# Optimization experiments

Hardware: AMD Instinct MI355X
Metric: run time of the kernel (lower is better)

## Reference

```python
import jax, jax.numpy as jnp
import numpy as np

B, S, D = 4, 2048, 2048
E = 8            # num_experts
TOP_K = 2
H = 1408         # intermediate_size per expert
SH = 2 * H       # shared expert intermediate (shared_experts=2)


def setup_inputs() -> dict:
    key = jax.random.key(0)
    ks = jax.random.split(key, 8)
    sc = 0.02
    return {
        "hidden_states": jax.random.normal(ks[0], (B, S, D), jnp.float32),
        "gate_w": jax.random.normal(ks[1], (E, D), jnp.float32) * sc,   # torch Linear weight [out,in]
        "w1": jax.random.normal(ks[2], (E, H, D), jnp.float32) * sc,    # gate_proj per expert
        "w3": jax.random.normal(ks[3], (E, H, D), jnp.float32) * sc,    # up_proj per expert
        "w2": jax.random.normal(ks[4], (E, D, H), jnp.float32) * sc,    # down_proj per expert
        "sw1": jax.random.normal(ks[5], (SH, D), jnp.float32) * sc,
        "sw3": jax.random.normal(ks[6], (SH, D), jnp.float32) * sc,
        "sw2": jax.random.normal(ks[7], (D, SH), jnp.float32) * sc,
    }


def reference(hidden_states, gate_w, w1, w3, w2, sw1, sw3, sw2):
    b, s, d = hidden_states.shape
    x = hidden_states.reshape(-1, d)                      # [T, D]
    logits = x @ gate_w.T                                 # [T, E]
    rw, sel = jax.lax.top_k(logits, TOP_K)                # [T, K]
    rw = jax.nn.softmax(rw, axis=-1)                      # norm_topk_prob=True
    onehot = jax.nn.one_hot(sel, E, dtype=x.dtype)        # [T, K, E]
    token_mask = onehot.sum(axis=1)                       # [T, E] in {0,1}
    # NOTE: faithful to the source quirk: expert_weights.sum(dim=-1) on a flat
    # masked gather sums routing weights over ALL tokens selecting the expert,
    # producing one scalar per expert.
    s_e = (rw[..., None] * onehot).sum(axis=(0, 1))       # [E]
    combine = token_mask * s_e                            # [T, E]
    # per-expert SwiGLU MLP on all tokens (dense combine form of gather/scatter)
    g = jnp.einsum('td,ehd->eth', x, w1)                  # [E, T, H]
    u = jnp.einsum('td,ehd->eth', x, w3)
    a = jax.nn.silu(g) * u
    y = jnp.einsum('eth,edh->etd', a, w2)                 # [E, T, D]
    out = jnp.einsum('te,etd->td', combine, y)            # [T, D]
    shared = (jax.nn.silu(x @ sw1.T) * (x @ sw3.T)) @ sw2.T
    out = out + shared
    return out.reshape(b, s, d)
```

## Files before the change

### kernel.cpp

```cpp
#include <hip/hip_runtime.h>
#include <hip/hip_bf16.h>
#include <stdint.h>

#define T_TOK 8192
#define DIM   2048
#define NEXP  8
#define HDIM  1408
#define SHDIM 2816

typedef __attribute__((ext_vector_type(8))) short bfrag;
typedef __attribute__((ext_vector_type(4))) float f32x4;

__device__ __forceinline__ short f2bf(float f) {
    union { float f; uint32_t u; } v; v.f = f;
    return (short)((v.u + 0x8000u) >> 16);
}

__device__ __forceinline__ bfrag cvt8(float4 a, float4 b) {
    bfrag r;
    r[0] = f2bf(a.x); r[1] = f2bf(a.y); r[2] = f2bf(a.z); r[3] = f2bf(a.w);
    r[4] = f2bf(b.x); r[5] = f2bf(b.y); r[6] = f2bf(b.z); r[7] = f2bf(b.w);
    return r;
}

__device__ __forceinline__ void gload16(const void* g, void* l) {
    __builtin_amdgcn_global_load_lds(
        (__attribute__((address_space(1))) void*)(g),
        (__attribute__((address_space(3))) void*)(l), 16, 0, 0);
}

#define MFMA16(a, b, c) __builtin_amdgcn_mfma_f32_16x16x32_bf16((a), (b), (c), 0, 0, 0)


__global__ __launch_bounds__(256) void gate_kernel(
    const float* __restrict__ x, const float* __restrict__ gw,
    int* __restrict__ sel, int* __restrict__ meta, float* __restrict__ s_e)
{
    __shared__ float g[NEXP * DIM];
    for (int i = threadIdx.x; i < NEXP * DIM; i += 256) g[i] = gw[i];
    __syncthreads();
    const int wid = threadIdx.x >> 6, lane = threadIdx.x & 63;
    for (int it = 0; it < 8; ++it) {
        const int t = blockIdx.x * 32 + wid * 8 + it;
        float acc[NEXP];
#pragma unroll
        for (int e = 0; e < NEXP; ++e) acc[e] = 0.f;
        const float4* xr = (const float4*)(x + (size_t)t * DIM);
        for (int j = 0; j < DIM / 4; j += 64) {
            float4 xv = xr[j + lane];
#pragma unroll
            for (int e = 0; e < NEXP; ++e) {
                float4 gv = *(const float4*)&g[e * DIM + (j + lane) * 4];
                acc[e] += xv.x * gv.x + xv.y * gv.y + xv.z * gv.z + xv.w * gv.w;
            }
        }
#pragma unroll
        for (int e = 0; e < NEXP; ++e)
            for (int o = 32; o; o >>= 1) acc[e] += __shfl_xor(acc[e], o);
        if (lane == 0) {
            int e0 = 0; float v0 = acc[0];
#pragma unroll
            for (int e = 1; e < NEXP; ++e) if (acc[e] > v0) { v0 = acc[e]; e0 = e; }
            int e1 = -1; float v1 = -3.4e38f;
#pragma unroll
            for (int e = 0; e < NEXP; ++e) if (e != e0 && acc[e] > v1) { v1 = acc[e]; e1 = e; }
            float p0 = 1.f / (1.f + __expf(v1 - v0));
            float p1 = 1.f - p0;
            sel[2 * t] = e0; sel[2 * t + 1] = e1;
            atomicAdd(&s_e[e0], p0); atomicAdd(&s_e[e1], p1);
            atomicAdd(&meta[e0], 1); atomicAdd(&meta[e1], 1);
        }
    }
}

__global__ void scan_kernel(int* meta) {
    if (threadIdx.x == 0) {
        int acc = 0;
        for (int e = 0; e < NEXP; ++e) {
            meta[16 + e] = acc;
            meta[8 + e]  = acc;
            acc += meta[e];
        }
        meta[24] = acc;
    }
}

__global__ __launch_bounds__(256) void fill_kernel(
    const int* __restrict__ sel, int* __restrict__ meta, int* __restrict__ list)
{
    const int t = blockIdx.x * 256 + threadIdx.x;
    int e0 = sel[2 * t], e1 = sel[2 * t + 1];
    int p0 = atomicAdd(&meta[8 + e0], 1); list[p0] = t;
    int p1 = atomicAdd(&meta[8 + e1], 1); list[p1] = t;
}

__global__ __launch_bounds__(256) void cvt_kernel(
    const float* __restrict__ in, __hip_bfloat16* __restrict__ out, int n8)
{
    int i = blockIdx.x * 256 + threadIdx.x;
    const int stride = gridDim.x * 256;
    for (; i < n8; i += stride) {
        const float4* p = (const float4*)(in + (size_t)i * 8);
        float4 a = p[0], b = p[1];
        *(bfrag*)(out + (size_t)i * 8) = cvt8(a, b);
    }
}


template<int N, bool GATHER>
__global__ __launch_bounds__(512, 2) void up_v3(
    const __hip_bfloat16* __restrict__ X,
    const __hip_bfloat16* __restrict__ W1,
    const __hip_bfloat16* __restrict__ W3,
    __hip_bfloat16* __restrict__ act,
    const int* __restrict__ list,
    const int* __restrict__ meta)
{
    constexpr int K = DIM;
    constexpr int NT = K / 64;
    constexpr int nx = N / 128, ny = T_TOK / 256, nz = GATHER ? NEXP : 1;
    constexpr int nwg = nx * ny * nz, cpx = nwg / 8;
    const int bid = (int)blockIdx.x + nx * ((int)blockIdx.y + ny * (int)blockIdx.z);
    const int virt = (bid & 7) * cpx + (bid >> 3);
    const int xi = virt % nx;
    const int rest = virt / nx;
    const int yi = rest % ny;
    const int e = rest / ny;

    int count, base;
    if (GATHER) {
        count = meta[e]; base = meta[16 + e];
        if (yi * 256 >= count) return;
    } else { count = T_TOK; base = 0; }
    const int m0 = yi * 256, n0 = xi * 128;

    __shared__ alignas(16) short As[2][256 * 64];
    __shared__ alignas(16) short B1s[2][128 * 64];
    __shared__ alignas(16) short B3s[2][128 * 64];

    const int tid = threadIdx.x, wid = tid >> 6, lane = tid & 63;
    const int rlo = lane >> 3;
    const int swslot = (lane & 7) ^ rlo;

    const __hip_bfloat16* pA[4];
#pragma unroll
    for (int q = 0; q < 4; ++q) {
        int row = (q * 8 + wid) * 8 + rlo;
        int r = m0 + row; if (r > count - 1) r = count - 1;
        int ga = GATHER ? list[base + r] : r;
        pA[q] = X + (size_t)ga * K + swslot * 8;
    }
    const __hip_bfloat16* pB1[2];
    const __hip_bfloat16* pB3[2];
#pragma unroll
    for (int q = 0; q < 2; ++q) {
        int row = (q * 8 + wid) * 8 + rlo;
        pB1[q] = W1 + ((size_t)e * N + n0 + row) * K + swslot * 8;
        pB3[q] = W3 + ((size_t)e * N + n0 + row) * K + swslot * 8;
    }

#define STAGE_UP(T, BUF) do { const int k0_ = (T) * 64;                         \
    _Pragma("unroll") for (int q = 0; q < 4; ++q)                               \
        gload16(pA[q] + k0_, &As[BUF][(q * 8 + wid) * 512]);                    \
    _Pragma("unroll") for (int q = 0; q < 2; ++q) {                             \
        gload16(pB1[q] + k0_, &B1s[BUF][(q * 8 + wid) * 512]);                  \
        gload16(pB3[q] + k0_, &B3s[BUF][(q * 8 + wid) * 512]); } } while (0)

    const int wm = wid >> 2, wn = wid & 3;
    const int l15 = lane & 15, lhi = lane >> 4;

    f32x4 accg[8][2], accu[8][2];
#pragma unroll
    for (int i = 0; i < 8; ++i)
#pragma unroll
        for (int j = 0; j < 2; ++j) { accg[i][j] = 0.f; accu[i][j] = 0.f; }

    STAGE_UP(0, 0);
    __syncthreads();
    int cur = 0;
#pragma unroll 1
    for (int t = 0; t < NT; ++t) {
        if (t + 1 < NT) STAGE_UP(t + 1, cur ^ 1);
        __builtin_amdgcn_sched_barrier(0);
        bfrag b1f[2][2], b3f[2][2];
#pragma unroll
        for (int j = 0; j < 2; ++j)
#pragma unroll
            for (int kk = 0; kk < 2; ++kk) {
                int rb = wn * 32 + j * 16 + l15;
                int c = kk * 4 + lhi;
                int off = rb * 128 + ((c ^ (rb & 7)) << 4);
                b1f[j][kk] = *(const bfrag*)((const char*)B1s[cur] + off);
                b3f[j][kk] = *(const bfrag*)((const char*)B3s[cur] + off);
            }
        __builtin_amdgcn_s_setprio(1);
#pragma unroll
        for (int i = 0; i < 8; ++i) {
            int ra = wm * 128 + i * 16 + l15;
            const char* abase = (const char*)As[cur] + ra * 128;
            bfrag a0 = *(const bfrag*)(abase + ((lhi       ^ (ra & 7)) << 4));
            bfrag a1 = *(const bfrag*)(abase + (((4 + lhi) ^ (ra & 7)) << 4));
#pragma unroll
            for (int j = 0; j < 2; ++j) {
                accg[i][j] = MFMA16(a0, b1f[j][0], accg[i][j]);
                accu[i][j] = MFMA16(a0, b3f[j][0], accu[i][j]);
                accg[i][j] = MFMA16(a1, b1f[j][1], accg[i][j]);
                accu[i][j] = MFMA16(a1, b3f[j][1], accu[i][j]);
            }
        }
        __builtin_amdgcn_s_setprio(0);
        __syncthreads();
        cur ^= 1;
    }
#undef STAGE_UP

#pragma unroll
    for (int i = 0; i < 8; ++i)
#pragma unroll
        for (int r = 0; r < 4; ++r) {
            int m = wm * 128 + i * 16 + lhi * 4 + r;
            if (m0 + m < count) {
#pragma unroll
                for (int j = 0; j < 2; ++j) {
                    float gg = accg[i][j][r];
                    float uu = accu[i][j][r];
                    float a = gg / (1.f + __expf(-gg)) * uu;
                    int n = n0 + wn * 32 + j * 16 + l15;
                    act[(size_t)(base + m0 + m) * N + n] = __float2bfloat16(a);
                }
            }
        }
}

template<int KD, bool SCATTER>
__global__ __launch_bounds__(512, 2) void down_v3(
    const __hip_bfloat16* __restrict__ A,
    const __hip_bfloat16* __restrict__ W2,
    float* __restrict__ out,
    const int* __restrict__ list,
    const int* __restrict__ meta,
    const float* __restrict__ s_e)
{
    constexpr int N = DIM;
    constexpr int NT = KD / 64;
    constexpr int nx = N / 256, ny = T_TOK / 256, nz = SCATTER ? NEXP : 1;
    constexpr int nwg = nx * ny * nz, cpx = nwg / 8;
    const int bid = (int)blockIdx.x + nx * ((int)blockIdx.y + ny * (int)blockIdx.z);
    const int virt = (bid & 7) * cpx + (bid >> 3);
    const int xi = virt % nx;
    const int rest = virt / nx;
    const int yi = rest % ny;
    const int e = rest / ny;

    int count, base;
    if (SCATTER) {
        count = meta[e]; base = meta[16 + e];
        if (yi * 256 >= count) return;
    } else { count = T_TOK; base = 0; }
    const int m0 = yi * 256, n0 = xi * 256;

    __shared__ alignas(16) short As[2][256 * 64];
    __shared__ alignas(16) short Bs[2][256 * 64];
    __shared__ int tok_s[256];

    const int tid = threadIdx.x, wid = tid >> 6, lane = tid & 63;
    if (SCATTER && tid < 256) {
        int r = m0 + tid; if (r > count - 1) r = count - 1;
        tok_s[tid] = list[base + r];
    }
    const int rlo = lane >> 3;
    const int swslot = (lane & 7) ^ rlo;

    const __hip_bfloat16* pA[4];
    const __hip_bfloat16* pB[4];
#pragma unroll
    for (int q = 0; q < 4; ++q) {
        int row = (q * 8 + wid) * 8 + rlo;
        int r = m0 + row; if (r > count - 1) r = count - 1;
        pA[q] = A  + (size_t)(base + r) * KD + swslot * 8;
        pB[q] = W2 + ((size_t)e * N + n0 + row) * KD + swslot * 8;
    }

#define STAGE_DN(T, BUF) do { const int k0_ = (T) * 64;                         \
    _Pragma("unroll") for (int q = 0; q < 4; ++q) {                             \
        gload16(pA[q] + k0_, &As[BUF][(q * 8 + wid) * 512]);                    \
        gload16(pB[q] + k0_, &Bs[BUF][(q * 8 + wid) * 512]); } } while (0)

    const int wm = wid >> 2, wn = wid & 3;
    const int l15 = lane & 15, lhi = lane >> 4;

    f32x4 acc[8][4];
#pragma unroll
    for (int i = 0; i < 8; ++i)
#pragma unroll
        for (int j = 0; j < 4; ++j) acc[i][j] = 0.f;

    STAGE_DN(0, 0);
    __syncthreads();
    int cur = 0;
#pragma unroll 1
    for (int t = 0; t < NT; ++t) {
        if (t + 1 < NT) STAGE_DN(t + 1, cur ^ 1);
        __builtin_amdgcn_sched_barrier(0);
        bfrag bf[4][2];
#pragma unroll
        for (int j = 0; j < 4; ++j)
#pragma unroll
            for (int kk = 0; kk < 2; ++kk) {
                int rb = wn * 64 + j * 16 + l15;
                int c = kk * 4 + lhi;
                bf[j][kk] = *(const bfrag*)((const char*)Bs[cur] + rb * 128 + ((c ^ (rb & 7)) << 4));
            }
        __builtin_amdgcn_s_setprio(1);
#pragma unroll
        for (int i = 0; i < 8; ++i) {
            int ra = wm * 128 + i * 16 + l15;
            const char* abase = (const char*)As[cur] + ra * 128;
            bfrag a0 = *(const bfrag*)(abase + ((lhi       ^ (ra & 7)) << 4));
            bfrag a1 = *(const bfrag*)(abase + (((4 + lhi) ^ (ra & 7)) << 4));
#pragma unroll
            for (int j = 0; j < 4; ++j) {
                acc[i][j] = MFMA16(a0, bf[j][0], acc[i][j]);
                acc[i][j] = MFMA16(a1, bf[j][1], acc[i][j]);
            }
        }
        __builtin_amdgcn_s_setprio(0);
        __syncthreads();
        cur ^= 1;
    }
#undef STAGE_DN

    const float scale = SCATTER ? s_e[e] : 1.0f;
#pragma unroll
    for (int i = 0; i < 8; ++i)
#pragma unroll
        for (int r = 0; r < 4; ++r) {
            int m = wm * 128 + i * 16 + lhi * 4 + r;
            if (m0 + m < count) {
#pragma unroll
                for (int j = 0; j < 4; ++j) {
                    int n = n0 + wn * 64 + j * 16 + l15;
                    float v = acc[i][j][r] * scale;
                    if (SCATTER) atomicAdd(&out[(size_t)tok_s[m] * DIM + n], v);
                    else         out[(size_t)(m0 + m) * DIM + n] = v;
                }
            }
        }
}

extern "C" void kernel_launch(void* const* d_in, const int* in_sizes, int n_in,
                              void* d_out, int out_size, void* d_ws, size_t ws_size,
                              hipStream_t stream) {
    const float* x   = (const float*)d_in[0];
    const float* gw  = (const float*)d_in[1];
    const float* w1  = (const float*)d_in[2];
    const float* w3  = (const float*)d_in[3];
    const float* w2  = (const float*)d_in[4];
    const float* sw1 = (const float*)d_in[5];
    const float* sw3 = (const float*)d_in[6];
    const float* sw2 = (const float*)d_in[7];
    float* out = (float*)d_out;

    const size_t SZ_X   = (size_t)T_TOK * DIM * 2;
    const size_t SZ_W   = (size_t)NEXP * HDIM * DIM * 2;
    const size_t SZ_SW  = (size_t)SHDIM * DIM * 2;
    const size_t SZ_ACT = (size_t)2 * T_TOK * HDIM * 2;
    const size_t need = SZ_X + 3 * SZ_W + 3 * SZ_SW + SZ_ACT
                      + (size_t)4 * T_TOK * sizeof(int) + 512;
    if (need > ws_size) return;

    char* p = (char*)d_ws;
    __hip_bfloat16* xbf   = (__hip_bfloat16*)p; p += SZ_X;
    __hip_bfloat16* w1bf  = (__hip_bfloat16*)p; p += SZ_W;
    __hip_bfloat16* w3bf  = (__hip_bfloat16*)p; p += SZ_W;
    __hip_bfloat16* w2bf  = (__hip_bfloat16*)p; p += SZ_W;
    __hip_bfloat16* sw1bf = (__hip_bfloat16*)p; p += SZ_SW;
    __hip_bfloat16* sw3bf = (__hip_bfloat16*)p; p += SZ_SW;
    __hip_bfloat16* sw2bf = (__hip_bfloat16*)p; p += SZ_SW;
    __hip_bfloat16* act   = (__hip_bfloat16*)p; p += SZ_ACT;
    int* list = (int*)p; p += (size_t)2 * T_TOK * sizeof(int);
    int* sel  = (int*)p; p += (size_t)2 * T_TOK * sizeof(int);
    int* meta = (int*)p;
    float* s_e = (float*)(meta + 32);

    hipMemsetAsync(meta, 0, 256, stream);
    gate_kernel<<<T_TOK / 32, 256, 0, stream>>>(x, gw, sel, meta, s_e);
    scan_kernel<<<1, 64, 0, stream>>>(meta);
    fill_kernel<<<T_TOK / 256, 256, 0, stream>>>(sel, meta, list);

    cvt_kernel<<<2048, 256, 0, stream>>>(x,   xbf,   T_TOK * DIM / 8);
    cvt_kernel<<<2048, 256, 0, stream>>>(w1,  w1bf,  NEXP * HDIM * DIM / 8);
    cvt_kernel<<<2048, 256, 0, stream>>>(w3,  w3bf,  NEXP * HDIM * DIM / 8);
    cvt_kernel<<<2048, 256, 0, stream>>>(w2,  w2bf,  NEXP * HDIM * DIM / 8);
    cvt_kernel<<<2048, 256, 0, stream>>>(sw1, sw1bf, SHDIM * DIM / 8);
    cvt_kernel<<<2048, 256, 0, stream>>>(sw3, sw3bf, SHDIM * DIM / 8);
    cvt_kernel<<<2048, 256, 0, stream>>>(sw2, sw2bf, SHDIM * DIM / 8);

    up_v3<SHDIM, false><<<dim3(SHDIM / 128, T_TOK / 256, 1), 512, 0, stream>>>(
        xbf, sw1bf, sw3bf, act, nullptr, meta);
    down_v3<SHDIM, false><<<dim3(DIM / 256, T_TOK / 256, 1), 512, 0, stream>>>(
        act, sw2bf, out, nullptr, meta, s_e);
    up_v3<HDIM, true><<<dim3(HDIM / 128, T_TOK / 256, NEXP), 512, 0, stream>>>(
        xbf, w1bf, w3bf, act, list, meta);
    down_v3<HDIM, true><<<dim3(DIM / 256, T_TOK / 256, NEXP), 512, 0, stream>>>(
        act, w2bf, out, list, meta, s_e);
}
```

Before: 1.181 ms.

## Fuse weight bf16 conversion into GEMM loads, replace atomic scatter with combine pass

Removes the separate fp32-to-bf16 conversion kernels. Activations are now converted inside the gate kernel, and weights are loaded as fp32 in the GEMM mainloops, converted in registers, and written to LDS after the MFMA block. The routed down-projection now writes bf16 per-slot outputs to a scratch buffer, and a new combine kernel applies the routing scales and adds both expert outputs per token in place of fp32 atomics. This saves the weight-conversion passes but doubles weight bytes read per tile (fp32) across many re-reads, adds register pressure, and replaces async LDS loads for B with synchronous ones.

```diff
diff --git a/kernel.cpp b/kernel.cpp
--- a/kernel.cpp
+++ b/kernel.cpp
@@ -10,10 +10,15 @@
 
 typedef __attribute__((ext_vector_type(8))) short bfrag;
 typedef __attribute__((ext_vector_type(4))) float f32x4;
+typedef __attribute__((ext_vector_type(4))) short s16x4;
 
 __device__ __forceinline__ short f2bf(float f) {
     union { float f; uint32_t u; } v; v.f = f;
     return (short)((v.u + 0x8000u) >> 16);
+}
+__device__ __forceinline__ float bf2f(short s) {
+    union { uint32_t u; float f; } v; v.u = ((uint32_t)(uint16_t)s) << 16;
+    return v.f;
 }
 
 __device__ __forceinline__ bfrag cvt8(float4 a, float4 b) {
@@ -34,6 +39,7 @@
 
 __global__ __launch_bounds__(256) void gate_kernel(
     const float* __restrict__ x, const float* __restrict__ gw,
+    __hip_bfloat16* __restrict__ xbf,
     int* __restrict__ sel, int* __restrict__ meta, float* __restrict__ s_e)
 {
     __shared__ float g[NEXP * DIM];
@@ -48,6 +54,8 @@
         const float4* xr = (const float4*)(x + (size_t)t * DIM);
         for (int j = 0; j < DIM / 4; j += 64) {
             float4 xv = xr[j + lane];
+            s16x4 xv16 = { f2bf(xv.x), f2bf(xv.y), f2bf(xv.z), f2bf(xv.w) };
+            *(s16x4*)&xbf[(size_t)t * DIM + (j + lane) * 4] = xv16;
 #pragma unroll
             for (int e = 0; e < NEXP; ++e) {
                 float4 gv = *(const float4*)&g[e * DIM + (j + lane) * 4];
@@ -86,32 +94,22 @@
 }
 
 __global__ __launch_bounds__(256) void fill_kernel(
-    const int* __restrict__ sel, int* __restrict__ meta, int* __restrict__ list)
+    const int* __restrict__ sel, int* __restrict__ meta,
+    int* __restrict__ list, int2* __restrict__ slots)
 {
     const int t = blockIdx.x * 256 + threadIdx.x;
     int e0 = sel[2 * t], e1 = sel[2 * t + 1];
     int p0 = atomicAdd(&meta[8 + e0], 1); list[p0] = t;
     int p1 = atomicAdd(&meta[8 + e1], 1); list[p1] = t;
-}
-
-__global__ __launch_bounds__(256) void cvt_kernel(
-    const float* __restrict__ in, __hip_bfloat16* __restrict__ out, int n8)
-{
-    int i = blockIdx.x * 256 + threadIdx.x;
-    const int stride = gridDim.x * 256;
-    for (; i < n8; i += stride) {
-        const float4* p = (const float4*)(in + (size_t)i * 8);
-        float4 a = p[0], b = p[1];
-        *(bfrag*)(out + (size_t)i * 8) = cvt8(a, b);
-    }
+    slots[t] = make_int2(p0, p1);
 }
 
 
 template<int N, bool GATHER>
-__global__ __launch_bounds__(512, 2) void up_v3(
+__global__ __launch_bounds__(512, 2) void up_v8(
     const __hip_bfloat16* __restrict__ X,
-    const __hip_bfloat16* __restrict__ W1,
-    const __hip_bfloat16* __restrict__ W3,
+    const float* __restrict__ W1,
+    const float* __restrict__ W3,
     __hip_bfloat16* __restrict__ act,
     const int* __restrict__ list,
     const int* __restrict__ meta)
@@ -150,21 +148,15 @@
         int ga = GATHER ? list[base + r] : r;
         pA[q] = X + (size_t)ga * K + swslot * 8;
     }
-    const __hip_bfloat16* pB1[2];
-    const __hip_bfloat16* pB3[2];
-#pragma unroll
-    for (int q = 0; q < 2; ++q) {
-        int row = (q * 8 + wid) * 8 + rlo;
-        pB1[q] = W1 + ((size_t)e * N + n0 + row) * K + swslot * 8;
-        pB3[q] = W3 + ((size_t)e * N + n0 + row) * K + swslot * 8;
-    }
-
-#define STAGE_UP(T, BUF) do { const int k0_ = (T) * 64;                         \
+    const int rb = tid >> 2, sq = tid & 3;
+    const float* pB1 = W1 + ((size_t)e * N + n0 + rb) * K + sq * 16;
+    const float* pB3 = W3 + ((size_t)e * N + n0 + rb) * K + sq * 16;
+    const int wb0 = rb * 128 + (((2 * sq)     ^ (rb & 7)) << 4);
+    const int wb1 = rb * 128 + (((2 * sq + 1) ^ (rb & 7)) << 4);
+
+#define STAGE_A(T, BUF) do { const int k0_ = (T) * 64;                          \
     _Pragma("unroll") for (int q = 0; q < 4; ++q)                               \
-        gload16(pA[q] + k0_, &As[BUF][(q * 8 + wid) * 512]);                    \
-    _Pragma("unroll") for (int q = 0; q < 2; ++q) {                             \
-        gload16(pB1[q] + k0_, &B1s[BUF][(q * 8 + wid) * 512]);                  \
-        gload16(pB3[q] + k0_, &B3s[BUF][(q * 8 + wid) * 512]); } } while (0)
+        gload16(pA[q] + k0_, &As[BUF][(q * 8 + wid) * 512]); } while (0)
 
     const int wm = wid >> 2, wn = wid & 3;
     const int l15 = lane & 15, lhi = lane >> 4;
@@ -175,21 +167,39 @@
 #pragma unroll
         for (int j = 0; j < 2; ++j) { accg[i][j] = 0.f; accu[i][j] = 0.f; }
 
-    STAGE_UP(0, 0);
+    {
+        const float4* s1 = (const float4*)pB1;
+        const float4* s3 = (const float4*)pB3;
+        float4 a0 = s1[0], a1 = s1[1], a2 = s1[2], a3 = s1[3];
+        float4 c0 = s3[0], c1 = s3[1], c2 = s3[2], c3 = s3[3];
+        *(bfrag*)((char*)B1s[0] + wb0) = cvt8(a0, a1);
+        *(bfrag*)((char*)B1s[0] + wb1) = cvt8(a2, a3);
+        *(bfrag*)((char*)B3s[0] + wb0) = cvt8(c0, c1);
+        *(bfrag*)((char*)B3s[0] + wb1) = cvt8(c2, c3);
+        STAGE_A(0, 0);
+    }
     __syncthreads();
     int cur = 0;
 #pragma unroll 1
     for (int t = 0; t < NT; ++t) {
-        if (t + 1 < NT) STAGE_UP(t + 1, cur ^ 1);
+        float4 a0, a1, a2, a3, c0, c1, c2, c3;
+        const bool pf = (t + 1 < NT);
+        if (pf) {
+            const float4* s1 = (const float4*)(pB1 + (t + 1) * 64);
+            const float4* s3 = (const float4*)(pB3 + (t + 1) * 64);
+            a0 = s1[0]; a1 = s1[1]; a2 = s1[2]; a3 = s1[3];
+            c0 = s3[0]; c1 = s3[1]; c2 = s3[2]; c3 = s3[3];
+            STAGE_A(t + 1, cur ^ 1);
+        }
         __builtin_amdgcn_sched_barrier(0);
         bfrag b1f[2][2], b3f[2][2];
 #pragma unroll
         for (int j = 0; j < 2; ++j)
 #pragma unroll
             for (int kk = 0; kk < 2; ++kk) {
-                int rb = wn * 32 + j * 16 + l15;
+                int rbr = wn * 32 + j * 16 + l15;
                 int c = kk * 4 + lhi;
-                int off = rb * 128 + ((c ^ (rb & 7)) << 4);
+                int off = rbr * 128 + ((c ^ (rbr & 7)) << 4);
                 b1f[j][kk] = *(const bfrag*)((const char*)B1s[cur] + off);
                 b3f[j][kk] = *(const bfrag*)((const char*)B3s[cur] + off);
             }
@@ -198,21 +208,27 @@
         for (int i = 0; i < 8; ++i) {
             int ra = wm * 128 + i * 16 + l15;
             const char* abase = (const char*)As[cur] + ra * 128;
-            bfrag a0 = *(const bfrag*)(abase + ((lhi       ^ (ra & 7)) << 4));
-            bfrag a1 = *(const bfrag*)(abase + (((4 + lhi) ^ (ra & 7)) << 4));
+            bfrag f0 = *(const bfrag*)(abase + ((lhi       ^ (ra & 7)) << 4));
+            bfrag f1 = *(const bfrag*)(abase + (((4 + lhi) ^ (ra & 7)) << 4));
 #pragma unroll
             for (int j = 0; j < 2; ++j) {
-                accg[i][j] = MFMA16(a0, b1f[j][0], accg[i][j]);
-                accu[i][j] = MFMA16(a0, b3f[j][0], accu[i][j]);
-                accg[i][j] = MFMA16(a1, b1f[j][1], accg[i][j]);
-                accu[i][j] = MFMA16(a1, b3f[j][1], accu[i][j]);
+                accg[i][j] = MFMA16(f0, b1f[j][0], accg[i][j]);
+                accu[i][j] = MFMA16(f0, b3f[j][0], accu[i][j]);
+                accg[i][j] = MFMA16(f1, b1f[j][1], accg[i][j]);
+                accu[i][j] = MFMA16(f1, b3f[j][1], accu[i][j]);
             }
         }
         __builtin_amdgcn_s_setprio(0);
+        if (pf) {
+            *(bfrag*)((char*)B1s[cur ^ 1] + wb0) = cvt8(a0, a1);
+            *(bfrag*)((char*)B1s[cur ^ 1] + wb1) = cvt8(a2, a3);
+            *(bfrag*)((char*)B3s[cur ^ 1] + wb0) = cvt8(c0, c1);
+            *(bfrag*)((char*)B3s[cur ^ 1] + wb1) = cvt8(c2, c3);
+        }
         __syncthreads();
         cur ^= 1;
     }
-#undef STAGE_UP
+#undef STAGE_A
 
 #pragma unroll
     for (int i = 0; i < 8; ++i)
@@ -232,18 +248,17 @@
         }
 }
 
-template<int KD, bool SCATTER>
-__global__ __launch_bounds__(512, 2) void down_v3(
+template<int KD, bool TO_BF16>
+__global__ __launch_bounds__(512, 2) void down_v8(
     const __hip_bfloat16* __restrict__ A,
-    const __hip_bfloat16* __restrict__ W2,
+    const float* __restrict__ W2,
     float* __restrict__ out,
-    const int* __restrict__ list,
-    const int* __restrict__ meta,
-    const float* __restrict__ s_e)
+    __hip_bfloat16* __restrict__ yscr,
+    const int* __restrict__ meta)
 {
     constexpr int N = DIM;
     constexpr int NT = KD / 64;
-    constexpr int nx = N / 256, ny = T_TOK / 256, nz = SCATTER ? NEXP : 1;
+    constexpr int nx = N / 256, ny = T_TOK / 256, nz = TO_BF16 ? NEXP : 1;
     constexpr int nwg = nx * ny * nz, cpx = nwg / 8;
     const int bid = (int)blockIdx.x + nx * ((int)blockIdx.y + ny * (int)blockIdx.z);
     const int virt = (bid & 7) * cpx + (bid >> 3);
@@ -253,7 +268,7 @@
     const int e = rest / ny;
 
     int count, base;
-    if (SCATTER) {
+    if (TO_BF16) {
         count = meta[e]; base = meta[16 + e];
         if (yi * 256 >= count) return;
     } else { count = T_TOK; base = 0; }
@@ -261,30 +276,28 @@
 
     __shared__ alignas(16) short As[2][256 * 64];
     __shared__ alignas(16) short Bs[2][256 * 64];
-    __shared__ int tok_s[256];
 
     const int tid = threadIdx.x, wid = tid >> 6, lane = tid & 63;
-    if (SCATTER && tid < 256) {
-        int r = m0 + tid; if (r > count - 1) r = count - 1;
-        tok_s[tid] = list[base + r];
-    }
     const int rlo = lane >> 3;
     const int swslot = (lane & 7) ^ rlo;
 
     const __hip_bfloat16* pA[4];
-    const __hip_bfloat16* pB[4];
 #pragma unroll
     for (int q = 0; q < 4; ++q) {
         int row = (q * 8 + wid) * 8 + rlo;
         int r = m0 + row; if (r > count - 1) r = count - 1;
-        pA[q] = A  + (size_t)(base + r) * KD + swslot * 8;
-        pB[q] = W2 + ((size_t)e * N + n0 + row) * KD + swslot * 8;
-    }
-
-#define STAGE_DN(T, BUF) do { const int k0_ = (T) * 64;                         \
-    _Pragma("unroll") for (int q = 0; q < 4; ++q) {                             \
-        gload16(pA[q] + k0_, &As[BUF][(q * 8 + wid) * 512]);                    \
-        gload16(pB[q] + k0_, &Bs[BUF][(q * 8 + wid) * 512]); } } while (0)
+        pA[q] = A + (size_t)(base + r) * KD + swslot * 8;
+    }
+    const int rb = tid >> 1, sq = tid & 1;
+    const float* pB = W2 + ((size_t)e * N + n0 + rb) * KD + sq * 32;
+    int wbB[4];
+#pragma unroll
+    for (int s = 0; s < 4; ++s)
+        wbB[s] = rb * 128 + (((4 * sq + s) ^ (rb & 7)) << 4);
+
+#define STAGE_A(T, BUF) do { const int k0_ = (T) * 64;                          \
+    _Pragma("unroll") for (int q = 0; q < 4; ++q)                               \
+        gload16(pA[q] + k0_, &As[BUF][(q * 8 + wid) * 512]); } while (0)
 
     const int wm = wid >> 2, wn = wid & 3;
     const int l15 = lane & 15, lhi = lane >> 4;
@@ -295,42 +308,61 @@
 #pragma unroll
         for (int j = 0; j < 4; ++j) acc[i][j] = 0.f;
 
-    STAGE_DN(0, 0);
+    {
+        const float4* s = (const float4*)pB;
+#pragma unroll
+        for (int h = 0; h < 4; ++h) {
+            float4 u0 = s[2 * h], u1 = s[2 * h + 1];
+            *(bfrag*)((char*)Bs[0] + wbB[h]) = cvt8(u0, u1);
+        }
+        STAGE_A(0, 0);
+    }
     __syncthreads();
     int cur = 0;
 #pragma unroll 1
     for (int t = 0; t < NT; ++t) {
-        if (t + 1 < NT) STAGE_DN(t + 1, cur ^ 1);
+        float4 u[8];
+        const bool pf = (t + 1 < NT);
+        if (pf) {
+            const float4* s = (const float4*)(pB + (t + 1) * 64);
+#pragma unroll
+            for (int h = 0; h < 8; ++h) u[h] = s[h];
+            STAGE_A(t + 1, cur ^ 1);
+        }
         __builtin_amdgcn_sched_barrier(0);
         bfrag bf[4][2];
 #pragma unroll
         for (int j = 0; j < 4; ++j)
 #pragma unroll
             for (int kk = 0; kk < 2; ++kk) {
-                int rb = wn * 64 + j * 16 + l15;
+                int rbr = wn * 64 + j * 16 + l15;
                 int c = kk * 4 + lhi;
-                bf[j][kk] = *(const bfrag*)((const char*)Bs[cur] + rb * 128 + ((c ^ (rb & 7)) << 4));
+                bf[j][kk] = *(const bfrag*)((const char*)Bs[cur] + rbr * 128 + ((c ^ (rbr & 7)) << 4));
             }
         __builtin_amdgcn_s_setprio(1);
 #pragma unroll
         for (int i = 0; i < 8; ++i) {
             int ra = wm * 128 + i * 16 + l15;
             const char* abase = (const char*)As[cur] + ra * 128;
-            bfrag a0 = *(const bfrag*)(abase + ((lhi       ^ (ra & 7)) << 4));
-            bfrag a1 = *(const bfrag*)(abase + (((4 + lhi) ^ (ra & 7)) << 4));
+            bfrag f0 = *(const bfrag*)(abase + ((lhi       ^ (ra & 7)) << 4));
+            bfrag f1 = *(const bfrag*)(abase + (((4 + lhi) ^ (ra & 7)) << 4));
 #pragma unroll
             for (int j = 0; j < 4; ++j) {
-                acc[i][j] = MFMA16(a0, bf[j][0], acc[i][j]);
-                acc[i][j] = MFMA16(a1, bf[j][1], acc[i][j]);
+                acc[i][j] = MFMA16(f0, bf[j][0], acc[i][j]);
+                acc[i][j] = MFMA16(f1, bf[j][1], acc[i][j]);
             }
         }
         __builtin_amdgcn_s_setprio(0);
+        if (pf) {
+#pragma unroll
+            for (int h = 0; h < 4; ++h)
+                *(bfrag*)((char*)Bs[cur ^ 1] + wbB[h]) = cvt8(u[2 * h], u[2 * h + 1]);
+        }
         __syncthreads();
         cur ^= 1;
     }
-#undef STAGE_DN
-
-    const float scale = SCATTER ? s_e[e] : 1.0f;
+#undef STAGE_A
+
 #pragma unroll
     for (int i = 0; i < 8; ++i)
 #pragma unroll
@@ -340,12 +372,38 @@
 #pragma unroll
                 for (int j = 0; j < 4; ++j) {
                     int n = n0 + wn * 64 + j * 16 + l15;
-                    float v = acc[i][j][r] * scale;
-                    if (SCATTER) atomicAdd(&out[(size_t)tok_s[m] * DIM + n], v);
-                    else         out[(size_t)(m0 + m) * DIM + n] = v;
+                    if (TO_BF16)
+                        yscr[(size_t)(base + m0 + m) * DIM + n] = __float2bfloat16(acc[i][j][r]);
+                    else
+                        out[(size_t)(m0 + m) * DIM + n] = acc[i][j][r];
                 }
             }
         }
+}
+
+__global__ __launch_bounds__(256) void combine_kernel(
+    float* __restrict__ out, const __hip_bfloat16* __restrict__ yscr,
+    const int* __restrict__ sel, const int2* __restrict__ slots,
+    const float* __restrict__ s_e)
+{
+    const int t = blockIdx.x;
+    const int d = threadIdx.x * 8;
+    const int2 sl = slots[t];
+    const float se0 = s_e[sel[2 * t]];
+    const float se1 = s_e[sel[2 * t + 1]];
+    bfrag y0 = *(const bfrag*)&yscr[(size_t)sl.x * DIM + d];
+    bfrag y1 = *(const bfrag*)&yscr[(size_t)sl.y * DIM + d];
+    float4* o = (float4*)(out + (size_t)t * DIM + d);
+    float4 o0 = o[0], o1 = o[1];
+    o0.x += se0 * bf2f(y0[0]) + se1 * bf2f(y1[0]);
+    o0.y += se0 * bf2f(y0[1]) + se1 * bf2f(y1[1]);
+    o0.z += se0 * bf2f(y0[2]) + se1 * bf2f(y1[2]);
+    o0.w += se0 * bf2f(y0[3]) + se1 * bf2f(y1[3]);
+    o1.x += se0 * bf2f(y0[4]) + se1 * bf2f(y1[4]);
+    o1.y += se0 * bf2f(y0[5]) + se1 * bf2f(y1[5]);
+    o1.z += se0 * bf2f(y0[6]) + se1 * bf2f(y1[6]);
+    o1.w += se0 * bf2f(y0[7]) + se1 * bf2f(y1[7]);
+    o[0] = o0; o[1] = o1;
 }
 
 extern "C" void kernel_launch(void* const* d_in, const int* in_sizes, int n_in,
@@ -362,46 +420,34 @@
     float* out = (float*)d_out;
 
     const size_t SZ_X   = (size_t)T_TOK * DIM * 2;
-    const size_t SZ_W   = (size_t)NEXP * HDIM * DIM * 2;
-    const size_t SZ_SW  = (size_t)SHDIM * DIM * 2;
     const size_t SZ_ACT = (size_t)2 * T_TOK * HDIM * 2;
-    const size_t need = SZ_X + 3 * SZ_W + 3 * SZ_SW + SZ_ACT
-                      + (size_t)4 * T_TOK * sizeof(int) + 512;
+    const size_t SZ_Y   = (size_t)2 * T_TOK * DIM * 2;
+    const size_t need = SZ_X + SZ_ACT + SZ_Y
+                      + (size_t)6 * T_TOK * sizeof(int) + 512;
     if (need > ws_size) return;
 
     char* p = (char*)d_ws;
-    __hip_bfloat16* xbf   = (__hip_bfloat16*)p; p += SZ_X;
-    __hip_bfloat16* w1bf  = (__hip_bfloat16*)p; p += SZ_W;
-    __hip_bfloat16* w3bf  = (__hip_bfloat16*)p; p += SZ_W;
-    __hip_bfloat16* w2bf  = (__hip_bfloat16*)p; p += SZ_W;
-    __hip_bfloat16* sw1bf = (__hip_bfloat16*)p; p += SZ_SW;
-    __hip_bfloat16* sw3bf = (__hip_bfloat16*)p; p += SZ_SW;
-    __hip_bfloat16* sw2bf = (__hip_bfloat16*)p; p += SZ_SW;
-    __hip_bfloat16* act   = (__hip_bfloat16*)p; p += SZ_ACT;
-    int* list = (int*)p; p += (size_t)2 * T_TOK * sizeof(int);
-    int* sel  = (int*)p; p += (size_t)2 * T_TOK * sizeof(int);
-    int* meta = (int*)p;
-    float* s_e = (float*)(meta + 32);
+    __hip_bfloat16* xbf  = (__hip_bfloat16*)p; p += SZ_X;
+    __hip_bfloat16* act  = (__hip_bfloat16*)p; p += SZ_ACT;
+    __hip_bfloat16* yscr = (__hip_bfloat16*)p; p += SZ_Y;
+    int*  list  = (int*)p;  p += (size_t)2 * T_TOK * sizeof(int);
+    int*  sel   = (int*)p;  p += (size_t)2 * T_TOK * sizeof(int);
+    int2* slots = (int2*)p; p += (size_t)2 * T_TOK * sizeof(int);
+    int*  meta  = (int*)p;
+    float* s_e  = (float*)(meta + 32);
 
     hipMemsetAsync(meta, 0, 256, stream);
-    gate_kernel<<<T_TOK / 32, 256, 0, stream>>>(x, gw, sel, meta, s_e);
+    gate_kernel<<<T_TOK / 32, 256, 0, stream>>>(x, gw, xbf, sel, meta, s_e);
     scan_kernel<<<1, 64, 0, stream>>>(meta);
-    fill_kernel<<<T_TOK / 256, 256, 0, stream>>>(sel, meta, list);
-
-    cvt_kernel<<<2048, 256, 0, stream>>>(x,   xbf,   T_TOK * DIM / 8);
-    cvt_kernel<<<2048, 256, 0, stream>>>(w1,  w1bf,  NEXP * HDIM * DIM / 8);
-    cvt_kernel<<<2048, 256, 0, stream>>>(w3,  w3bf,  NEXP * HDIM * DIM / 8);
-    cvt_kernel<<<2048, 256, 0, stream>>>(w2,  w2bf,  NEXP * HDIM * DIM / 8);
-    cvt_kernel<<<2048, 256, 0, stream>>>(sw1, sw1bf, SHDIM * DIM / 8);
-    cvt_kernel<<<2048, 256, 0, stream>>>(sw3, sw3bf, SHDIM * DIM / 8);
-    cvt_kernel<<<2048, 256, 0, stream>>>(sw2, sw2bf, SHDIM * DIM / 8);
-
-    up_v3<SHDIM, false><<<dim3(SHDIM / 128, T_TOK / 256, 1), 512, 0, stream>>>(
-        xbf, sw1bf, sw3bf, act, nullptr, meta);
-    down_v3<SHDIM, false><<<dim3(DIM / 256, T_TOK / 256, 1), 512, 0, stream>>>(
-        act, sw2bf, out, nullptr, meta, s_e);
-    up_v3<HDIM, true><<<dim3(HDIM / 128, T_TOK / 256, NEXP), 512, 0, stream>>>(
-        xbf, w1bf, w3bf, act, list, meta);
-    down_v3<HDIM, true><<<dim3(DIM / 256, T_TOK / 256, NEXP), 512, 0, stream>>>(
-        act, w2bf, out, list, meta, s_e);
-}
+    fill_kernel<<<T_TOK / 256, 256, 0, stream>>>(sel, meta, list, slots);
+
+    up_v8<SHDIM, false><<<dim3(SHDIM / 128, T_TOK / 256, 1), 512, 0, stream>>>(
+        xbf, sw1, sw3, act, nullptr, meta);
+    down_v8<SHDIM, false><<<dim3(DIM / 256, T_TOK / 256, 1), 512, 0, stream>>>(
+        act, sw2, out, nullptr, meta);
+    up_v8<HDIM, true><<<dim3(HDIM / 128, T_TOK / 256, NEXP), 512, 0, stream>>>(
+        xbf, w1, w3, act, list, meta);
+    down_v8<HDIM, true><<<dim3(DIM / 256, T_TOK / 256, NEXP), 512, 0, stream>>>(
+        act, w2, out, yscr, meta);
+    combine_kernel<<<T_TOK, 256, 0, stream>>>(out, yscr, sel, slots, s_e);
+}
```

Measured after the change: 1.385 ms. +17.3%, slower.

## Merge shared/expert GEMM launches, fuse conversions, replace atomic scatter with combine

Applied to the files above, without the earlier changes.

The x-to-bf16 conversion moves into the gate kernel, and the w1/w3/sw1/sw3 conversions become a single launch. The w2/sw2 conversions run as extra workgroups inside the merged up-projection kernel. Shared-expert and routed-expert tiles now share one up launch and one down launch when the workspace allows it. The routed down-projection no longer does fp32 atomicAdd scatter into the output: it writes bf16 per-slot results to a scratch buffer that reuses the w1/w3 bf16 space, and a new combine kernel adds the two scaled expert contributions per token. This removes launch tails, atomic contention and separate conversion passes, at the cost of extra scratch traffic, bf16 rounding of expert outputs, and runtime branching in the GEMM kernels.

```diff
diff --git a/kernel.cpp b/kernel.cpp
--- a/kernel.cpp
+++ b/kernel.cpp
@@ -10,10 +10,15 @@
 
 typedef __attribute__((ext_vector_type(8))) short bfrag;
 typedef __attribute__((ext_vector_type(4))) float f32x4;
+typedef __attribute__((ext_vector_type(4))) short s16x4;
 
 __device__ __forceinline__ short f2bf(float f) {
     union { float f; uint32_t u; } v; v.f = f;
     return (short)((v.u + 0x8000u) >> 16);
+}
+__device__ __forceinline__ float bf2f(short s) {
+    union { uint32_t u; float f; } v; v.u = ((uint32_t)(uint16_t)s) << 16;
+    return v.f;
 }
 
 __device__ __forceinline__ bfrag cvt8(float4 a, float4 b) {
@@ -34,6 +39,7 @@
 
 __global__ __launch_bounds__(256) void gate_kernel(
     const float* __restrict__ x, const float* __restrict__ gw,
+    __hip_bfloat16* __restrict__ xbf,
     int* __restrict__ sel, int* __restrict__ meta, float* __restrict__ s_e)
 {
     __shared__ float g[NEXP * DIM];
@@ -48,6 +54,8 @@
         const float4* xr = (const float4*)(x + (size_t)t * DIM);
         for (int j = 0; j < DIM / 4; j += 64) {
             float4 xv = xr[j + lane];
+            s16x4 xv16 = { f2bf(xv.x), f2bf(xv.y), f2bf(xv.z), f2bf(xv.w) };
+            *(s16x4*)&xbf[(size_t)t * DIM + (j + lane) * 4] = xv16;
 #pragma unroll
             for (int e = 0; e < NEXP; ++e) {
                 float4 gv = *(const float4*)&g[e * DIM + (j + lane) * 4];
@@ -86,59 +94,98 @@
 }
 
 __global__ __launch_bounds__(256) void fill_kernel(
-    const int* __restrict__ sel, int* __restrict__ meta, int* __restrict__ list)
+    const int* __restrict__ sel, int* __restrict__ meta,
+    int* __restrict__ list, int2* __restrict__ slots)
 {
     const int t = blockIdx.x * 256 + threadIdx.x;
     int e0 = sel[2 * t], e1 = sel[2 * t + 1];
     int p0 = atomicAdd(&meta[8 + e0], 1); list[p0] = t;
     int p1 = atomicAdd(&meta[8 + e1], 1); list[p1] = t;
-}
-
-__global__ __launch_bounds__(256) void cvt_kernel(
-    const float* __restrict__ in, __hip_bfloat16* __restrict__ out, int n8)
-{
-    int i = blockIdx.x * 256 + threadIdx.x;
+    slots[t] = make_int2(p0, p1);
+}
+
+#define D1 2883584
+#define D2 5767168
+#define D3 6488064
+#define D4 7208960
+__global__ __launch_bounds__(256) void cvt4_kernel(
+    const float* __restrict__ s0, const float* __restrict__ s1,
+    const float* __restrict__ s2, const float* __restrict__ s3,
+    __hip_bfloat16* __restrict__ d0, __hip_bfloat16* __restrict__ d1,
+    __hip_bfloat16* __restrict__ d2, __hip_bfloat16* __restrict__ d3)
+{
     const int stride = gridDim.x * 256;
-    for (; i < n8; i += stride) {
-        const float4* p = (const float4*)(in + (size_t)i * 8);
+    for (int i = blockIdx.x * 256 + threadIdx.x; i < D4; i += stride) {
+        const float* s; __hip_bfloat16* d; int off;
+        if      (i < D1) { s = s0; d = d0; off = i; }
+        else if (i < D2) { s = s1; d = d1; off = i - D1; }
+        else if (i < D3) { s = s2; d = d2; off = i - D2; }
+        else             { s = s3; d = d3; off = i - D3; }
+        const float4* p = (const float4*)(s + (size_t)off * 8);
         float4 a = p[0], b = p[1];
-        *(bfrag*)(out + (size_t)i * 8) = cvt8(a, b);
-    }
-}
-
-
-template<int N, bool GATHER>
-__global__ __launch_bounds__(512, 2) void up_v3(
+        *(bfrag*)(d + (size_t)off * 8) = cvt8(a, b);
+    }
+}
+
+#define W2ELEMS 23068672
+#define CVTCHUNKS 7040
+
+__global__ __launch_bounds__(512, 2) void up_merged(
     const __hip_bfloat16* __restrict__ X,
-    const __hip_bfloat16* __restrict__ W1,
-    const __hip_bfloat16* __restrict__ W3,
-    __hip_bfloat16* __restrict__ act,
-    const int* __restrict__ list,
-    const int* __restrict__ meta)
+    const __hip_bfloat16* __restrict__ W1,  const __hip_bfloat16* __restrict__ W3,
+    const __hip_bfloat16* __restrict__ SW1, const __hip_bfloat16* __restrict__ SW3,
+    __hip_bfloat16* __restrict__ act_sh,
+    __hip_bfloat16* __restrict__ act_ex,
+    const int* __restrict__ list, const int* __restrict__ meta,
+    const float* __restrict__ w2f, const float* __restrict__ sw2f,
+    __hip_bfloat16* __restrict__ w2bf, __hip_bfloat16* __restrict__ sw2bf,
+    int ns, int ne, int ncvt)
 {
     constexpr int K = DIM;
     constexpr int NT = K / 64;
-    constexpr int nx = N / 128, ny = T_TOK / 256, nz = GATHER ? NEXP : 1;
-    constexpr int nwg = nx * ny * nz, cpx = nwg / 8;
-    const int bid = (int)blockIdx.x + nx * ((int)blockIdx.y + ny * (int)blockIdx.z);
+    const int tid = threadIdx.x, bid = blockIdx.x;
+
+    if (bid >= ns + ne) {
+        for (int c = bid - (ns + ne); c < CVTCHUNKS; c += ncvt) {
+            size_t elem = (size_t)c * 4096 + tid * 8;
+            const float* s; __hip_bfloat16* d;
+            if (elem < W2ELEMS) { s = w2f + elem; d = w2bf + elem; }
+            else { s = sw2f + (elem - W2ELEMS); d = sw2bf + (elem - W2ELEMS); }
+            float4 a = ((const float4*)s)[0], b = ((const float4*)s)[1];
+            *(bfrag*)d = cvt8(a, b);
+        }
+        return;
+    }
+
+    const int cpx = (ns + ne) >> 3;
     const int virt = (bid & 7) * cpx + (bid >> 3);
-    const int xi = virt % nx;
-    const int rest = virt / nx;
-    const int yi = rest % ny;
-    const int e = rest / ny;
-
-    int count, base;
-    if (GATHER) {
+
+    int N, n0, m0, count, base;
+    const __hip_bfloat16 *B1p, *B3p;
+    __hip_bfloat16* actp;
+    bool gather;
+    if (virt < ns) {
+        N = SHDIM; gather = false;
+        n0 = (virt % 22) * 128; m0 = (virt / 22) * 256;
+        count = T_TOK; base = 0;
+        B1p = SW1; B3p = SW3; actp = act_sh;
+    } else {
+        const int t = virt - ns;
+        const int e = t / 352, r = t % 352;
+        N = HDIM; gather = true;
+        n0 = (r % 11) * 128; m0 = (r / 11) * 256;
         count = meta[e]; base = meta[16 + e];
-        if (yi * 256 >= count) return;
-    } else { count = T_TOK; base = 0; }
-    const int m0 = yi * 256, n0 = xi * 128;
+        if (m0 >= count) return;
+        B1p = W1 + (size_t)e * HDIM * K;
+        B3p = W3 + (size_t)e * HDIM * K;
+        actp = act_ex;
+    }
 
     __shared__ alignas(16) short As[2][256 * 64];
     __shared__ alignas(16) short B1s[2][128 * 64];
     __shared__ alignas(16) short B3s[2][128 * 64];
 
-    const int tid = threadIdx.x, wid = tid >> 6, lane = tid & 63;
+    const int wid = tid >> 6, lane = tid & 63;
     const int rlo = lane >> 3;
     const int swslot = (lane & 7) ^ rlo;
 
@@ -147,7 +194,7 @@
     for (int q = 0; q < 4; ++q) {
         int row = (q * 8 + wid) * 8 + rlo;
         int r = m0 + row; if (r > count - 1) r = count - 1;
-        int ga = GATHER ? list[base + r] : r;
+        int ga = gather ? list[base + r] : r;
         pA[q] = X + (size_t)ga * K + swslot * 8;
     }
     const __hip_bfloat16* pB1[2];
@@ -155,8 +202,8 @@
 #pragma unroll
     for (int q = 0; q < 2; ++q) {
         int row = (q * 8 + wid) * 8 + rlo;
-        pB1[q] = W1 + ((size_t)e * N + n0 + row) * K + swslot * 8;
-        pB3[q] = W3 + ((size_t)e * N + n0 + row) * K + swslot * 8;
+        pB1[q] = B1p + (size_t)(n0 + row) * K + swslot * 8;
+        pB3[q] = B3p + (size_t)(n0 + row) * K + swslot * 8;
     }
 
 #define STAGE_UP(T, BUF) do { const int k0_ = (T) * 64;                         \
@@ -226,48 +273,47 @@
                     float uu = accu[i][j][r];
                     float a = gg / (1.f + __expf(-gg)) * uu;
                     int n = n0 + wn * 32 + j * 16 + l15;
-                    act[(size_t)(base + m0 + m) * N + n] = __float2bfloat16(a);
+                    actp[(size_t)(base + m0 + m) * N + n] = __float2bfloat16(a);
                 }
             }
         }
 }
 
-template<int KD, bool SCATTER>
-__global__ __launch_bounds__(512, 2) void down_v3(
-    const __hip_bfloat16* __restrict__ A,
-    const __hip_bfloat16* __restrict__ W2,
-    float* __restrict__ out,
-    const int* __restrict__ list,
-    const int* __restrict__ meta,
-    const float* __restrict__ s_e)
+__global__ __launch_bounds__(512, 2) void down_merged(
+    const __hip_bfloat16* __restrict__ act_sh,
+    const __hip_bfloat16* __restrict__ act_ex,
+    const __hip_bfloat16* __restrict__ W2, const __hip_bfloat16* __restrict__ SW2,
+    float* __restrict__ out, __hip_bfloat16* __restrict__ yscr,
+    const int* __restrict__ meta, int ns, int ne)
 {
     constexpr int N = DIM;
-    constexpr int NT = KD / 64;
-    constexpr int nx = N / 256, ny = T_TOK / 256, nz = SCATTER ? NEXP : 1;
-    constexpr int nwg = nx * ny * nz, cpx = nwg / 8;
-    const int bid = (int)blockIdx.x + nx * ((int)blockIdx.y + ny * (int)blockIdx.z);
+    const int tid = threadIdx.x, bid = blockIdx.x;
+    const int cpx = (ns + ne) >> 3;
     const int virt = (bid & 7) * cpx + (bid >> 3);
-    const int xi = virt % nx;
-    const int rest = virt / nx;
-    const int yi = rest % ny;
-    const int e = rest / ny;
-
-    int count, base;
-    if (SCATTER) {
+
+    int KD, n0, m0, count, base;
+    const __hip_bfloat16 *Ap, *Bp;
+    bool tobf;
+    if (virt < ns) {
+        KD = SHDIM; tobf = false;
+        n0 = (virt % 8) * 256; m0 = (virt / 8) * 256;
+        count = T_TOK; base = 0;
+        Ap = act_sh; Bp = SW2;
+    } else {
+        const int t = virt - ns;
+        const int e = t / 256, r = t % 256;
+        KD = HDIM; tobf = true;
+        n0 = (r % 8) * 256; m0 = (r / 8) * 256;
         count = meta[e]; base = meta[16 + e];
-        if (yi * 256 >= count) return;
-    } else { count = T_TOK; base = 0; }
-    const int m0 = yi * 256, n0 = xi * 256;
+        if (m0 >= count) return;
+        Ap = act_ex; Bp = W2 + (size_t)e * N * HDIM;
+    }
+    const int NT = KD / 64;
 
     __shared__ alignas(16) short As[2][256 * 64];
     __shared__ alignas(16) short Bs[2][256 * 64];
-    __shared__ int tok_s[256];
-
-    const int tid = threadIdx.x, wid = tid >> 6, lane = tid & 63;
-    if (SCATTER && tid < 256) {
-        int r = m0 + tid; if (r > count - 1) r = count - 1;
-        tok_s[tid] = list[base + r];
-    }
+
+    const int wid = tid >> 6, lane = tid & 63;
     const int rlo = lane >> 3;
     const int swslot = (lane & 7) ^ rlo;
 
@@ -277,8 +323,8 @@
     for (int q = 0; q < 4; ++q) {
         int row = (q * 8 + wid) * 8 + rlo;
         int r = m0 + row; if (r > count - 1) r = count - 1;
-        pA[q] = A  + (size_t)(base + r) * KD + swslot * 8;
-        pB[q] = W2 + ((size_t)e * N + n0 + row) * KD + swslot * 8;
+        pA[q] = Ap + (size_t)(base + r) * KD + swslot * 8;
+        pB[q] = Bp + (size_t)(n0 + row) * KD + swslot * 8;
     }
 
 #define STAGE_DN(T, BUF) do { const int k0_ = (T) * 64;                         \
@@ -330,7 +376,6 @@
     }
 #undef STAGE_DN
 
-    const float scale = SCATTER ? s_e[e] : 1.0f;
 #pragma unroll
     for (int i = 0; i < 8; ++i)
 #pragma unroll
@@ -340,12 +385,38 @@
 #pragma unroll
                 for (int j = 0; j < 4; ++j) {
                     int n = n0 + wn * 64 + j * 16 + l15;
-                    float v = acc[i][j][r] * scale;
-                    if (SCATTER) atomicAdd(&out[(size_t)tok_s[m] * DIM + n], v);
-                    else         out[(size_t)(m0 + m) * DIM + n] = v;
+                    if (tobf)
+                        yscr[(size_t)(base + m0 + m) * DIM + n] = __float2bfloat16(acc[i][j][r]);
+                    else
+                        out[(size_t)(m0 + m) * DIM + n] = acc[i][j][r];
                 }
             }
         }
+}
+
+__global__ __launch_bounds__(256) void combine_kernel(
+    float* __restrict__ out, const __hip_bfloat16* __restrict__ yscr,
+    const int* __restrict__ sel, const int2* __restrict__ slots,
+    const float* __restrict__ s_e)
+{
+    const int t = blockIdx.x;
+    const int d = threadIdx.x * 8;
+    const int2 sl = slots[t];
+    const float se0 = s_e[sel[2 * t]];
+    const float se1 = s_e[sel[2 * t + 1]];
+    bfrag y0 = *(const bfrag*)&yscr[(size_t)sl.x * DIM + d];
+    bfrag y1 = *(const bfrag*)&yscr[(size_t)sl.y * DIM + d];
+    float4* o = (float4*)(out + (size_t)t * DIM + d);
+    float4 o0 = o[0], o1 = o[1];
+    o0.x += se0 * bf2f(y0[0]) + se1 * bf2f(y1[0]);
+    o0.y += se0 * bf2f(y0[1]) + se1 * bf2f(y1[1]);
+    o0.z += se0 * bf2f(y0[2]) + se1 * bf2f(y1[2]);
+    o0.w += se0 * bf2f(y0[3]) + se1 * bf2f(y1[3]);
+    o1.x += se0 * bf2f(y0[4]) + se1 * bf2f(y1[4]);
+    o1.y += se0 * bf2f(y0[5]) + se1 * bf2f(y1[5]);
+    o1.z += se0 * bf2f(y0[6]) + se1 * bf2f(y1[6]);
+    o1.w += se0 * bf2f(y0[7]) + se1 * bf2f(y1[7]);
+    o[0] = o0; o[1] = o1;
 }
 
 extern "C" void kernel_launch(void* const* d_in, const int* in_sizes, int n_in,
@@ -361,13 +432,15 @@
     const float* sw2 = (const float*)d_in[7];
     float* out = (float*)d_out;
 
-    const size_t SZ_X   = (size_t)T_TOK * DIM * 2;
-    const size_t SZ_W   = (size_t)NEXP * HDIM * DIM * 2;
-    const size_t SZ_SW  = (size_t)SHDIM * DIM * 2;
-    const size_t SZ_ACT = (size_t)2 * T_TOK * HDIM * 2;
-    const size_t need = SZ_X + 3 * SZ_W + 3 * SZ_SW + SZ_ACT
-                      + (size_t)4 * T_TOK * sizeof(int) + 512;
-    if (need > ws_size) return;
+    const size_t SZ_X    = (size_t)T_TOK * DIM * 2;
+    const size_t SZ_W    = (size_t)NEXP * HDIM * DIM * 2;
+    const size_t SZ_SW   = (size_t)SHDIM * DIM * 2;
+    const size_t SZ_ACTS = (size_t)T_TOK * SHDIM * 2;
+    const size_t SZ_ACTE = (size_t)2 * T_TOK * HDIM * 2;
+    const size_t SZ_INTS = (size_t)6 * T_TOK * sizeof(int) + 512;
+
+    const size_t need_base   = SZ_X + 3 * SZ_W + 3 * SZ_SW + SZ_ACTS + SZ_INTS;
+    const size_t need_merged = need_base + SZ_ACTE;
 
     char* p = (char*)d_ws;
     __hip_bfloat16* xbf   = (__hip_bfloat16*)p; p += SZ_X;
@@ -377,31 +450,44 @@
     __hip_bfloat16* sw1bf = (__hip_bfloat16*)p; p += SZ_SW;
     __hip_bfloat16* sw3bf = (__hip_bfloat16*)p; p += SZ_SW;
     __hip_bfloat16* sw2bf = (__hip_bfloat16*)p; p += SZ_SW;
-    __hip_bfloat16* act   = (__hip_bfloat16*)p; p += SZ_ACT;
-    int* list = (int*)p; p += (size_t)2 * T_TOK * sizeof(int);
-    int* sel  = (int*)p; p += (size_t)2 * T_TOK * sizeof(int);
-    int* meta = (int*)p;
-    float* s_e = (float*)(meta + 32);
+    __hip_bfloat16* act_sh = (__hip_bfloat16*)p; p += SZ_ACTS;
+    const bool merged = (need_merged <= ws_size);
+    __hip_bfloat16* act_ex = merged ? (__hip_bfloat16*)p : act_sh;
+    if (merged) p += SZ_ACTE;
+    int*  list  = (int*)p;  p += (size_t)2 * T_TOK * sizeof(int);
+    int*  sel   = (int*)p;  p += (size_t)2 * T_TOK * sizeof(int);
+    int2* slots = (int2*)p; p += (size_t)2 * T_TOK * sizeof(int);
+    int*  meta  = (int*)p;
+    float* s_e  = (float*)(meta + 32);
+    __hip_bfloat16* yscr = w1bf;
+    if (need_base > ws_size) return;
 
     hipMemsetAsync(meta, 0, 256, stream);
-    gate_kernel<<<T_TOK / 32, 256, 0, stream>>>(x, gw, sel, meta, s_e);
+    gate_kernel<<<T_TOK / 32, 256, 0, stream>>>(x, gw, xbf, sel, meta, s_e);
     scan_kernel<<<1, 64, 0, stream>>>(meta);
-    fill_kernel<<<T_TOK / 256, 256, 0, stream>>>(sel, meta, list);
-
-    cvt_kernel<<<2048, 256, 0, stream>>>(x,   xbf,   T_TOK * DIM / 8);
-    cvt_kernel<<<2048, 256, 0, stream>>>(w1,  w1bf,  NEXP * HDIM * DIM / 8);
-    cvt_kernel<<<2048, 256, 0, stream>>>(w3,  w3bf,  NEXP * HDIM * DIM / 8);
-    cvt_kernel<<<2048, 256, 0, stream>>>(w2,  w2bf,  NEXP * HDIM * DIM / 8);
-    cvt_kernel<<<2048, 256, 0, stream>>>(sw1, sw1bf, SHDIM * DIM / 8);
-    cvt_kernel<<<2048, 256, 0, stream>>>(sw3, sw3bf, SHDIM * DIM / 8);
-    cvt_kernel<<<2048, 256, 0, stream>>>(sw2, sw2bf, SHDIM * DIM / 8);
-
-    up_v3<SHDIM, false><<<dim3(SHDIM / 128, T_TOK / 256, 1), 512, 0, stream>>>(
-        xbf, sw1bf, sw3bf, act, nullptr, meta);
-    down_v3<SHDIM, false><<<dim3(DIM / 256, T_TOK / 256, 1), 512, 0, stream>>>(
-        act, sw2bf, out, nullptr, meta, s_e);
-    up_v3<HDIM, true><<<dim3(HDIM / 128, T_TOK / 256, NEXP), 512, 0, stream>>>(
-        xbf, w1bf, w3bf, act, list, meta);
-    down_v3<HDIM, true><<<dim3(DIM / 256, T_TOK / 256, NEXP), 512, 0, stream>>>(
-        act, w2bf, out, list, meta, s_e);
-}
+    fill_kernel<<<T_TOK / 256, 256, 0, stream>>>(sel, meta, list, slots);
+    cvt4_kernel<<<2048, 256, 0, stream>>>(w1, w3, sw1, sw3, w1bf, w3bf, sw1bf, sw3bf);
+
+    const int NS_U = 704, NE_U = 2816, NCVT = 220;
+    const int NS_D = 256, NE_D = 2048;
+
+    if (merged) {
+        up_merged<<<NS_U + NE_U + NCVT, 512, 0, stream>>>(
+            xbf, w1bf, w3bf, sw1bf, sw3bf, act_sh, act_ex, list, meta,
+            w2, sw2, w2bf, sw2bf, NS_U, NE_U, NCVT);
+        down_merged<<<NS_D + NE_D, 512, 0, stream>>>(
+            act_sh, act_ex, w2bf, sw2bf, out, yscr, meta, NS_D, NE_D);
+    } else {
+        up_merged<<<NS_U + NCVT, 512, 0, stream>>>(
+            xbf, w1bf, w3bf, sw1bf, sw3bf, act_sh, act_ex, list, meta,
+            w2, sw2, w2bf, sw2bf, NS_U, 0, NCVT);
+        down_merged<<<NS_D, 512, 0, stream>>>(
+            act_sh, act_ex, w2bf, sw2bf, out, yscr, meta, NS_D, 0);
+        up_merged<<<NE_U, 512, 0, stream>>>(
+            xbf, w1bf, w3bf, sw1bf, sw3bf, act_sh, act_ex, list, meta,
+            w2, sw2, w2bf, sw2bf, 0, NE_U, 0);
+        down_merged<<<NE_D, 512, 0, stream>>>(
+            act_sh, act_ex, w2bf, sw2bf, out, yscr, meta, 0, NE_D);
+    }
+    combine_kernel<<<T_TOK, 256, 0, stream>>>(out, yscr, sel, slots, s_e);
+}
```

Result: slower. 2.134 ms (+80.8%).
